# Performance work log

Measured on AMD Instinct MI355X. Metric: run time of the kernel, lower is better.

## Reference

```python
import jax, jax.numpy as jnp
import numpy as np

N = 100000      # num nodes
E = 400000      # num edges (avg degree 4, AIG-like sparse DAG)
NVT = 7         # node type count (one-hot)
VHS = 100       # vertex hidden size
CHS = 30        # clause hidden size
SV = 512        # number of state-variable nodes
NROUNDS = 8     # message passing rounds


def setup_inputs() -> dict:
    key = jax.random.key(0)
    ks = jax.random.split(key, 40)
    s = 0.08  # ~1/sqrt(VHS), matches torch default uniform scale

    def mat(k, shape):
        return jax.random.normal(k, shape, jnp.float32) * s

    edge_index = jax.random.randint(ks[0], (2, E), 0, N)
    sv_node = jax.random.randint(ks[1], (SV,), 0, N)
    types = jax.random.randint(ks[2], (N,), 0, NVT)
    x = jax.nn.one_hot(types, NVT, dtype=jnp.float32)  # [N, NVT]
    ones_e = jnp.ones((E,), jnp.float32)
    # degrees used as divisors after SpMM (clamped >= 1 like real graphs w/ self edges)
    ind = jnp.clip(jax.ops.segment_sum(ones_e, edge_index[1], num_segments=N), 1.0, None)
    outd = jnp.clip(jax.ops.segment_sum(ones_e, edge_index[0], num_segments=N), 1.0, None)

    inp = {
        "x": x, "edge_index": edge_index, "sv_node": sv_node,
        "ind": ind, "outd": outd, "n_clause": 1, "pretrain_round": 1,
        # type init vectors: Linear(1,VHS)(ones(1)) == weight[:,0] + bias, one row per type
        "type_vec": mat(ks[3], (NVT, VHS)),
        # forward_msg MLP
        "fm_w1": mat(ks[4], (VHS, VHS)), "fm_b1": mat(ks[5], (VHS,)),
        "fm_w2": mat(ks[6], (VHS, VHS)), "fm_b2": mat(ks[7], (VHS,)),
        "fm_w3": mat(ks[8], (VHS, VHS)), "fm_b3": mat(ks[9], (VHS,)),
        # backward_msg MLP
        "bm_w1": mat(ks[10], (VHS, VHS)), "bm_b1": mat(ks[11], (VHS,)),
        "bm_w2": mat(ks[12], (VHS, VHS)), "bm_b2": mat(ks[13], (VHS,)),
        "bm_w3": mat(ks[14], (VHS, VHS)), "bm_b3": mat(ks[15], (VHS,)),
        # forward_update GRU (gates ordered r,z,n as in torch)
        "fg_wih": mat(ks[16], (VHS, 3 * VHS)), "fg_whh": mat(ks[17], (VHS, 3 * VHS)),
        "fg_bih": mat(ks[18], (3 * VHS,)), "fg_bhh": mat(ks[19], (3 * VHS,)),
        # backward_update GRU
        "bg_wih": mat(ks[20], (VHS, 3 * VHS)), "bg_whh": mat(ks[21], (VHS, 3 * VHS)),
        "bg_bih": mat(ks[22], (3 * VHS,)), "bg_bhh": mat(ks[23], (3 * VHS,)),
        # sv_feature_pretrain_layer
        "pw1": mat(ks[24], (VHS, CHS)), "pb1": mat(ks[25], (CHS,)),
        "pw2": mat(ks[26], (CHS, 1)), "pb2": mat(ks[27], (1,)),
    }
    return inp


def reference(x, edge_index, sv_node, ind, outd, n_clause, pretrain_round,
              type_vec, fm_w1, fm_b1, fm_w2, fm_b2, fm_w3, fm_b3,
              bm_w1, bm_b1, bm_w2, bm_b2, bm_w3, bm_b3,
              fg_wih, fg_whh, fg_bih, fg_bhh,
              bg_wih, bg_whh, bg_bih, bg_bhh,
              pw1, pb1, pw2, pb2):
    n = x.shape[0]
    src, dst = edge_index[0], edge_index[1]
    ind_c = ind[:, None]   # [N,1]
    outd_c = outd[:, None]

    def mlp(h, w1, b1, w2, b2, w3, b3):
        h = jax.nn.relu(h @ w1 + b1)
        h = jax.nn.relu(h @ w2 + b2)
        return h @ w3 + b3

    def gru(xin, h, wih, whh, bih, bhh):
        # single-step torch GRU: r,z,n gate ordering
        gi = xin @ wih + bih
        gh = h @ whh + bhh
        ir, iz, ig = jnp.split(gi, 3, axis=-1)
        hr, hz, hg = jnp.split(gh, 3, axis=-1)
        r = jax.nn.sigmoid(ir + hr)
        z = jax.nn.sigmoid(iz + hz)
        g = jnp.tanh(ig + r * hg)
        return (1.0 - z) * g + z * h

    def round_fn(vs, _):
        # forward direction: adj_fwd[dst, src] -> aggregate msgs from src into dst
        m = mlp(vs, fm_w1, fm_b1, fm_w2, fm_b2, fm_w3, fm_b3)
        fwd = jax.ops.segment_sum(m[src], dst, num_segments=n) / ind_c
        vs = gru(fwd, vs, fg_wih, fg_whh, fg_bih, fg_bhh)
        # backward direction: adj_bwd[src, dst] -> aggregate msgs from dst into src
        m = mlp(vs, bm_w1, bm_b1, bm_w2, bm_b2, bm_w3, bm_b3)
        bwd = jax.ops.segment_sum(m[dst], src, num_segments=n) / outd_c
        vs = gru(bwd, vs, bg_wih, bg_whh, bg_bih, bg_bhh)
        return vs, None

    vs0 = x @ type_vec  # [N, VHS]
    vs, _ = jax.lax.scan(jax.checkpoint(round_fn), vs0, None, length=NROUNDS)

    # pretrain_round branch: sv_feature_pretrain_layer(var_state[sv_node]).t()[0]
    shortcut = vs[sv_node]  # [SV, VHS]
    h = jax.nn.relu(shortcut @ pw1 + pb1)
    return (h @ pw2 + pb2)[:, 0]  # [SV]
```

## Files before the change

### kernel.cpp

```cpp
#include <hip/hip_runtime.h>
#include <math.h>

#define NVTC 7
#define VHS 100
#define CHS 30
#define LDP 112
#define CTW 128
#define WFRAG_SZ 32768

typedef short short8 __attribute__((ext_vector_type(8)));
typedef float floatx4 __attribute__((ext_vector_type(4)));

#define MFMA(a, b, c) __builtin_amdgcn_mfma_f32_16x16x32_bf16((a), (b), (c), 0, 0, 0)

#define GLOAD16(g, l)                                                              \
  __builtin_amdgcn_global_load_lds((const __attribute__((address_space(1))) void*)(g), \
                                   (__attribute__((address_space(3))) void*)(l), 16, 0, 0)

__device__ __forceinline__ unsigned short f2bf(float f) {
  unsigned u = __float_as_uint(f);
  return (unsigned short)((u + 0x7fffu + ((u >> 16) & 1u)) >> 16);
}
__device__ __forceinline__ float bf2f(unsigned short h) {
  return __uint_as_float((unsigned)h << 16);
}
__device__ __forceinline__ float sigmf(float v) { return 1.f / (1.f + expf(-v)); }


__global__ void zero_int_kernel(int* __restrict__ p, int n) {
  int i = blockIdx.x * 256 + threadIdx.x;
  if (i < n) p[i] = 0;
}

__global__ void inv_kernel(const float* __restrict__ ind, const float* __restrict__ outd,
                           float* __restrict__ inv_ind, float* __restrict__ inv_outd, int n) {
  int i = blockIdx.x * 256 + threadIdx.x;
  if (i < n) { inv_ind[i] = 1.0f / ind[i]; inv_outd[i] = 1.0f / outd[i]; }
}

__global__ void wfrag_kernel(const float* __restrict__ src, int srcLD, int colOff,
                             short* __restrict__ dst) {
  int t = blockIdx.x * 256 + threadIdx.x;
  if (t >= 2048) return;
  int lane = t & 63, rest = t >> 6;
  int ct = rest & 7, kc = rest >> 3;
  int col = ct * 16 + (lane & 15);
  int kbase = kc * 32 + (lane >> 4) * 8;
  short8 hv, lv;
  #pragma unroll
  for (int i = 0; i < 8; ++i) {
    int k = kbase + i;
    float v = (k < VHS && col < VHS) ? src[(size_t)k * srcLD + colOff + col] : 0.f;
    unsigned short h16 = f2bf(v);
    hv[i] = (short)h16;
    lv[i] = (short)f2bf(v - bf2f(h16));
  }
  int base = ((kc * 8 + ct) * 2 * 64 + lane) * 8;
  *(short8*)(dst + base)       = hv;
  *(short8*)(dst + base + 512) = lv;
}

__global__ void pad_b_kernel(const float* __restrict__ b1, int off1,
                             const float* b2, int off2, float* __restrict__ dst) {
  int c = threadIdx.x;
  float v = 0.f;
  if (c < VHS) { v = b1[off1 + c]; if (b2) v += b2[off2 + c]; }
  dst[c] = v;
}

__global__ void init_vs_kernel(const float* __restrict__ x, const float* __restrict__ tv,
                               char* __restrict__ vsp, int N) {
  int node = blockIdx.x, c = threadIdx.x;
  if (node >= N) return;
  float v = 0.f;
  if (c < VHS) {
    #pragma unroll
    for (int t = 0; t < NVTC; ++t) v += x[(size_t)node * NVTC + t] * tv[t * VHS + c];
  }
  unsigned short hi = f2bf(v);
  unsigned short lo = f2bf(v - bf2f(hi));
  char* rowp = vsp + ((size_t)node << 9);
  *(unsigned short*)(rowp + 2 * c)       = hi;
  *(unsigned short*)(rowp + 256 + 2 * c) = lo;
}


__global__ void hist_kernel(const int* __restrict__ ei, int E, int* hin, int* hout) {
  int e = blockIdx.x * 256 + threadIdx.x;
  if (e < E) {
    atomicAdd(&hout[ei[e]], 1);
    atomicAdd(&hin[ei[E + e]], 1);
  }
}

__global__ void scan_block_kernel(const int* __restrict__ in, int* __restrict__ mid,
                                  int* __restrict__ sums, int n) {
  __shared__ int lds[256];
  int tid = threadIdx.x;
  int base = blockIdx.x * 1024 + tid * 4;
  int v0 = (base + 0 < n) ? in[base + 0] : 0;
  int v1 = (base + 1 < n) ? in[base + 1] : 0;
  int v2 = (base + 2 < n) ? in[base + 2] : 0;
  int v3 = (base + 3 < n) ? in[base + 3] : 0;
  int s = v0 + v1 + v2 + v3;
  lds[tid] = s;
  __syncthreads();
  for (int off = 1; off < 256; off <<= 1) {
    int t = (tid >= off) ? lds[tid - off] : 0;
    __syncthreads();
    lds[tid] += t;
    __syncthreads();
  }
  int excl = lds[tid] - s;
  int e0 = excl + v0, e1 = e0 + v1, e2 = e1 + v2, e3 = e2 + v3;
  if (base + 0 < n) mid[base + 0] = e0;
  if (base + 1 < n) mid[base + 1] = e1;
  if (base + 2 < n) mid[base + 2] = e2;
  if (base + 3 < n) mid[base + 3] = e3;
  if (tid == 255) sums[blockIdx.x] = lds[255];
}

__global__ void scan_sums_kernel(int* sums, int nb) {
  __shared__ int lds[256];
  int tid = threadIdx.x;
  int v = (tid < nb) ? sums[tid] : 0;
  lds[tid] = v;
  __syncthreads();
  for (int off = 1; off < 256; off <<= 1) {
    int t = (tid >= off) ? lds[tid - off] : 0;
    __syncthreads();
    lds[tid] += t;
    __syncthreads();
  }
  if (tid < nb) sums[tid] = lds[tid];
}

__global__ void scan_finalize_kernel(const int* __restrict__ mid, const int* __restrict__ sums,
                                     int* __restrict__ rp, int n) {
  int i = blockIdx.x * 256 + threadIdx.x;
  if (i >= n) return;
  int blk = i >> 10;
  int add = (blk > 0) ? sums[blk - 1] : 0;
  rp[i + 1] = mid[i] + add;
  if (i == 0) rp[0] = 0;
}

__global__ void fill_kernel(const int* __restrict__ ei, int E, int gOff, int sOff,
                            const int* __restrict__ rp, int* cnt, int* col) {
  int e = blockIdx.x * 256 + threadIdx.x;
  if (e >= E) return;
  int v = ei[sOff + e];
  int p = rp[v] + atomicAdd(&cnt[v], 1);
  col[p] = ei[gOff + e];
}

__global__ void sort_rows_kernel(const int* __restrict__ rp, int* col, int n) {
  int v = blockIdx.x * 256 + threadIdx.x;
  if (v >= n) return;
  int a = rp[v], b = rp[v + 1];
  for (int i = a + 1; i < b; ++i) {
    int key = col[i];
    int j = i - 1;
    while (j >= a && col[j] > key) { col[j + 1] = col[j]; --j; }
    col[j + 1] = key;
  }
}

__global__ void __launch_bounds__(256)
gather_kernel(const float* __restrict__ m, const int* __restrict__ rp,
              const int* __restrict__ col, const float* __restrict__ iv,
              char* __restrict__ aggp, int N) {
  int v = blockIdx.x * 8 + (threadIdx.x >> 5);
  if (v >= N) return;
  int lane = threadIdx.x & 31;
  char* rowp = aggp + ((size_t)v << 9);
  if (lane < 28) {
    float4 a = make_float4(0.f, 0.f, 0.f, 0.f);
    int s = rp[v], e = rp[v + 1];
    for (int i = s; i < e; ++i) {
      float4 u = ((const float4*)(m + (size_t)col[i] * LDP))[lane];
      a.x += u.x; a.y += u.y; a.z += u.z; a.w += u.w;
    }
    const float sc = iv[v];
    a.x *= sc; a.y *= sc; a.z *= sc; a.w *= sc;
    unsigned short h0 = f2bf(a.x), h1 = f2bf(a.y), h2 = f2bf(a.z), h3 = f2bf(a.w);
    unsigned short l0 = f2bf(a.x - bf2f(h0)), l1 = f2bf(a.y - bf2f(h1));
    unsigned short l2 = f2bf(a.z - bf2f(h2)), l3 = f2bf(a.w - bf2f(h3));
    *(uint2*)(rowp + 8 * lane) =
        make_uint2((unsigned)h0 | ((unsigned)h1 << 16), (unsigned)h2 | ((unsigned)h3 << 16));
    *(uint2*)(rowp + 256 + 8 * lane) =
        make_uint2((unsigned)l0 | ((unsigned)l1 << 16), (unsigned)l2 | ((unsigned)l3 << 16));
  } else {
    *(uint2*)(rowp + 8 * lane)       = make_uint2(0u, 0u);
    *(uint2*)(rowp + 256 + 8 * lane) = make_uint2(0u, 0u);
  }
}

__global__ void __launch_bounds__(256, 2)
mlp3_kernel(const char* __restrict__ vsp,
            const short* __restrict__ W1f, const short* __restrict__ W2f,
            const short* __restrict__ W3f,
            const float* __restrict__ b1, const float* __restrict__ b2,
            const float* __restrict__ b3, float* __restrict__ OUT, int N) {
  __shared__ __align__(16) char lds[65536];
  char* ldsH = lds;
  char* ldsL = lds + 16384;
  const int lane = threadIdx.x & 63, wave = threadIdx.x >> 6;
  const int lrbase = wave * 16;
  const int row0 = blockIdx.x * 64 + lrbase;
  const int a_r = lane & 15, a_kg = lane >> 4;
  const int col_l = lane & 15;

  short8 Fh[4], Fl[4];
  {
    const char* vrow = vsp + (((size_t)(row0 + a_r)) << 9) + (a_kg << 4);
    #pragma unroll
    for (int kc = 0; kc < 4; ++kc) {
      Fh[kc] = *(const short8*)(vrow + kc * 64);
      Fl[kc] = *(const short8*)(vrow + 256 + kc * 64);
    }
  }
  float B1[7], B2[7], B3[7];
  #pragma unroll
  for (int ct = 0; ct < 7; ++ct) {
    const int k = ct * 16 + col_l;
    B1[ct] = b1[k]; B2[ct] = b2[k]; B3[ct] = b3[k];
  }
  if (lane < 32) {
    int row = lrbase + (lane >> 1), sl = 14 + (lane & 1);
    int byte = row * 256 + ((sl * 16) ^ ((row & 7) << 4));
    short8 z = {0, 0, 0, 0, 0, 0, 0, 0};
    *(short8*)(ldsH + byte) = z;
    *(short8*)(ldsL + byte) = z;
  }
  asm volatile("s_waitcnt vmcnt(0)" ::: "memory");

  floatx4 acc[7];
  #pragma unroll
  for (int c = 0; c < 7; ++c) acc[c] = (floatx4){0.f, 0.f, 0.f, 0.f};

#define MSTAGE(WF, KC, BOFF)                                                   \
  {                                                                            \
    _Pragma("unroll") for (int q = 0; q < 4; ++q) {                            \
      const int c_ = wave * 4 + q;                                             \
      GLOAD16((const char*)(WF) + (size_t)((KC) * 16384 + c_ * 1024) + lane * 16, \
              lds + (BOFF) + c_ * 1024);                                       \
    }                                                                          \
  }

#define MCOMP(KC, BOFF, VA)                                                    \
  {                                                                            \
    asm volatile("s_waitcnt vmcnt(" VA ")" ::: "memory");                      \
    __builtin_amdgcn_s_barrier();                                              \
    short8 wt[14];                                                             \
    _Pragma("unroll") for (int c = 0; c < 7; ++c) {                            \
      wt[2 * c]     = *(const short8*)(lds + (BOFF) + (2 * c) * 1024 + lane * 16); \
      wt[2 * c + 1] = *(const short8*)(lds + (BOFF) + (2 * c + 1) * 1024 + lane * 16); \
    }                                                                          \
    __builtin_amdgcn_s_setprio(1);                                             \
    _Pragma("unroll") for (int c = 0; c < 7; ++c) {                            \
      acc[c] = MFMA(Fh[KC], wt[2 * c], acc[c]);                                \
      acc[c] = MFMA(Fh[KC], wt[2 * c + 1], acc[c]);                            \
      acc[c] = MFMA(Fl[KC], wt[2 * c], acc[c]);                                \
    }                                                                          \
    __builtin_amdgcn_s_setprio(0);                                             \
    __builtin_amdgcn_sched_barrier(0);                                         \
    __builtin_amdgcn_s_barrier();                                              \
  }

  auto wbrelu = [&](const float* B) {
    const int rloc0 = lrbase + (lane >> 4) * 4;
    #pragma unroll
    for (int ct = 0; ct < 7; ++ct) {
      int k = ct * 16 + col_l;
      #pragma unroll
      for (int j = 0; j < 4; ++j) {
        int row = rloc0 + j;
        float v = fmaxf(acc[ct][j] + B[ct], 0.f);
        unsigned short h16 = f2bf(v);
        unsigned short l16 = f2bf(v - bf2f(h16));
        int byte = row * 256 + ((k * 2) ^ ((row & 7) << 4));
        *(short*)(ldsH + byte) = (short)h16;
        *(short*)(ldsL + byte) = (short)l16;
      }
      acc[ct] = (floatx4){0.f, 0.f, 0.f, 0.f};
    }
  };
  auto ldfrags = [&]() {
    #pragma unroll
    for (int kc = 0; kc < 4; ++kc) {
      int r = lrbase + a_r;
      int byte = r * 256 + ((((kc * 4 + a_kg) * 16)) ^ ((r & 7) << 4));
      Fh[kc] = *(const short8*)(ldsH + byte);
      Fl[kc] = *(const short8*)(ldsL + byte);
    }
  };

  MSTAGE(W1f, 0, 32768) MSTAGE(W1f, 1, 49152)
  MCOMP(0, 32768, "4")  MSTAGE(W1f, 2, 32768)
  MCOMP(1, 49152, "4")  MSTAGE(W1f, 3, 49152)
  MCOMP(2, 32768, "4")  MSTAGE(W2f, 0, 32768)
  MCOMP(3, 49152, "4")  MSTAGE(W2f, 1, 49152)
  wbrelu(B1); ldfrags();
  MCOMP(0, 32768, "4")  MSTAGE(W2f, 2, 32768)
  MCOMP(1, 49152, "4")  MSTAGE(W2f, 3, 49152)
  MCOMP(2, 32768, "4")  MSTAGE(W3f, 0, 32768)
  MCOMP(3, 49152, "4")  MSTAGE(W3f, 1, 49152)
  wbrelu(B2); ldfrags();
  MCOMP(0, 32768, "4")  MSTAGE(W3f, 2, 32768)
  MCOMP(1, 49152, "4")  MSTAGE(W3f, 3, 49152)
  MCOMP(2, 32768, "4")
  MCOMP(3, 49152, "0")

  const int r0 = row0 + (lane >> 4) * 4;
  #pragma unroll
  for (int ct = 0; ct < 7; ++ct) {
    const int c = ct * 16 + col_l;
    #pragma unroll
    for (int j = 0; j < 4; ++j) {
      const int r = r0 + j;
      if (r < N) OUT[(size_t)r * LDP + c] = acc[ct][j] + B3[ct];
    }
  }
#undef MSTAGE
#undef MCOMP
}

__global__ void __launch_bounds__(256, 2)
gru_kernel(const char* __restrict__ aggp, const char* __restrict__ vsp,
           const short* __restrict__ Wbase,
           const float* __restrict__ br, const float* __restrict__ bz,
           const float* __restrict__ big, const float* __restrict__ bhg,
           char* __restrict__ outp, int N) {
  __shared__ __align__(16) char wlds[49152];
  const int lane = threadIdx.x & 63, wave = threadIdx.x >> 6;
  const int row0 = blockIdx.x * 64 + wave * 16;
  const int a_r = lane & 15;
  const int kgo = (lane >> 4) << 4;
  const int col_l = lane & 15;
  const int jr0 = row0 + (lane >> 4) * 4;

  short8 Ah[4], Al[4], Vh[4], Vl[4];
  {
    const char* arow = aggp + (((size_t)(row0 + a_r)) << 9) + kgo;
    const char* vrow = vsp  + (((size_t)(row0 + a_r)) << 9) + kgo;
    #pragma unroll
    for (int kc = 0; kc < 4; ++kc) {
      Ah[kc] = *(const short8*)(arow + kc * 64);
      Al[kc] = *(const short8*)(arow + 256 + kc * 64);
      Vh[kc] = *(const short8*)(vrow + kc * 64);
      Vl[kc] = *(const short8*)(vrow + 256 + kc * 64);
    }
  }
  float ho[7][4];
  #pragma unroll
  for (int ct = 0; ct < 7; ++ct) {
    const int ccol = ct * 16 + col_l;
    #pragma unroll
    for (int j = 0; j < 4; ++j) {
      const char* hrow = vsp + ((size_t)(jr0 + j) << 9);
      ho[ct][j] = bf2f(*(const unsigned short*)(hrow + 2 * ccol)) +
                  bf2f(*(const unsigned short*)(hrow + 256 + 2 * ccol));
    }
  }
  float bR[7], bZ[7], bI[7], bH[7];
  #pragma unroll
  for (int ct = 0; ct < 7; ++ct) {
    const int ccol = ct * 16 + col_l;
    bR[ct] = br[ccol]; bZ[ct] = bz[ccol]; bI[ct] = big[ccol]; bH[ct] = bhg[ccol];
  }
  asm volatile("s_waitcnt vmcnt(0)" ::: "memory");

#define GRU_STAGE(CT, KH, BOFF)                                                \
  {                                                                            \
    _Pragma("unroll") for (int q = 0; q < 6; ++q) {                            \
      const int c_ = wave * 6 + q;                                             \
      const int m_ = c_ >> 2, kcl_ = (c_ >> 1) & 1, p_ = c_ & 1;               \
      const size_t gb_ = (size_t)m_ * 65536 +                                  \
          (size_t)(((((KH) * 2 + kcl_) * 8 + (CT)) * 2048) + p_ * 1024);       \
      GLOAD16((const char*)Wbase + gb_ + lane * 16, wlds + (BOFF) + c_ * 1024);\
    }                                                                          \
  }

#define GRU_HALF(KH, BOFF)                                                     \
  {                                                                            \
    _Pragma("unroll") for (int kcl = 0; kcl < 2; ++kcl) {                      \
      const int kc_ = (KH) * 2 + kcl;                                          \
      short8 wt[12];                                                           \
      _Pragma("unroll") for (int mp = 0; mp < 12; ++mp) {                      \
        const int m_ = mp >> 1, p_ = mp & 1;                                   \
        const int chunk_ = m_ * 4 + kcl * 2 + p_;                              \
        wt[mp] = *(const short8*)(wlds + (BOFF) + chunk_ * 1024 + lane * 16);  \
      }                                                                        \
      __builtin_amdgcn_s_setprio(1);                                           \
      rc = MFMA(Ah[kc_], wt[0], rc);  rc = MFMA(Ah[kc_], wt[1], rc);  rc = MFMA(Al[kc_], wt[0], rc); \
      zc = MFMA(Ah[kc_], wt[2], zc);  zc = MFMA(Ah[kc_], wt[3], zc);  zc = MFMA(Al[kc_], wt[2], zc); \
      ic = MFMA(Ah[kc_], wt[4], ic);  ic = MFMA(Ah[kc_], wt[5], ic);  ic = MFMA(Al[kc_], wt[4], ic); \
      rc = MFMA(Vh[kc_], wt[6], rc);  rc = MFMA(Vh[kc_], wt[7], rc);  rc = MFMA(Vl[kc_], wt[6], rc); \
      zc = MFMA(Vh[kc_], wt[8], zc);  zc = MFMA(Vh[kc_], wt[9], zc);  zc = MFMA(Vl[kc_], wt[8], zc); \
      hc = MFMA(Vh[kc_], wt[10], hc); hc = MFMA(Vh[kc_], wt[11], hc); hc = MFMA(Vl[kc_], wt[10], hc); \
      __builtin_amdgcn_s_setprio(0);                                           \
    }                                                                          \
  }

#define GRU_ITER(CT, VA, VB, STG)                                              \
  {                                                                            \
    floatx4 rc = {0.f, 0.f, 0.f, 0.f};                                         \
    floatx4 zc = {0.f, 0.f, 0.f, 0.f};                                         \
    floatx4 ic = {0.f, 0.f, 0.f, 0.f};                                         \
    floatx4 hc = {0.f, 0.f, 0.f, 0.f};                                         \
    asm volatile("s_waitcnt vmcnt(" VA ")" ::: "memory");                      \
    __builtin_amdgcn_s_barrier();                                              \
    GRU_HALF(0, 0)                                                             \
    __builtin_amdgcn_sched_barrier(0);                                         \
    __builtin_amdgcn_s_barrier();                                              \
    if (STG) GRU_STAGE((CT) + 1, 0, 0)                                         \
    asm volatile("s_waitcnt vmcnt(" VB ")" ::: "memory");                      \
    __builtin_amdgcn_s_barrier();                                              \
    GRU_HALF(1, 24576)                                                         \
    __builtin_amdgcn_sched_barrier(0);                                         \
    __builtin_amdgcn_s_barrier();                                              \
    if (STG) GRU_STAGE((CT) + 1, 1, 24576)                                     \
    const float brv = bR[CT], bzv = bZ[CT], bigv = bI[CT], bhgv = bH[CT];      \
    const int ccol = (CT) * 16 + col_l;                                        \
    _Pragma("unroll") for (int j = 0; j < 4; ++j) {                            \
      const float rv = sigmf(rc[j] + brv);                                     \
      const float zv = sigmf(zc[j] + bzv);                                     \
      const float gv = tanhf(ic[j] + bigv + rv * (hc[j] + bhgv));              \
      const float v = (1.f - zv) * gv + zv * ho[CT][j];                        \
      const unsigned short hi = f2bf(v);                                       \
      const unsigned short lo = f2bf(v - bf2f(hi));                            \
      char* orow = outp + ((size_t)(jr0 + j) << 9);                            \
      *(unsigned short*)(orow + 2 * ccol)       = hi;                          \
      *(unsigned short*)(orow + 256 + 2 * ccol) = lo;                          \
    }                                                                          \
  }

  GRU_STAGE(0, 0, 0)
  GRU_STAGE(0, 1, 24576)

  GRU_ITER(0, "6",  "6",  1)
  GRU_ITER(1, "14", "14", 1)
  GRU_ITER(2, "14", "14", 1)
  GRU_ITER(3, "14", "14", 1)
  GRU_ITER(4, "14", "14", 1)
  GRU_ITER(5, "14", "14", 1)
  GRU_ITER(6, "14", "8",  0)

#undef GRU_STAGE
#undef GRU_HALF
#undef GRU_ITER
}

__global__ void final_kernel(const char* __restrict__ vsp, const int* __restrict__ sv,
                             const float* __restrict__ pw1, const float* __restrict__ pb1,
                             const float* __restrict__ pw2, const float* __restrict__ pb2,
                             float* __restrict__ out, int SVn) {
  int b = blockIdx.x;
  if (b >= SVn) return;
  int tid = threadIdx.x;
  int node = sv[b];
  const char* rowp = vsp + ((size_t)node << 9);
  float p = 0.f;
  if (tid < CHS) {
    float acc = 0.f;
    for (int k = 0; k < VHS; ++k) {
      float xv = bf2f(*(const unsigned short*)(rowp + 2 * k)) +
                 bf2f(*(const unsigned short*)(rowp + 256 + 2 * k));
      acc += xv * pw1[k * CHS + tid];
    }
    float h = fmaxf(acc + pb1[tid], 0.f);
    p = h * pw2[tid];
  }
  #pragma unroll
  for (int off = 32; off > 0; off >>= 1) p += __shfl_down(p, off);
  if (tid == 0) out[b] = p + pb2[0];
}

extern "C" void kernel_launch(void* const* d_in, const int* in_sizes, int n_in,
                              void* d_out, int out_size, void* d_ws, size_t ws_size,
                              hipStream_t stream) {
  const float* x      = (const float*)d_in[0];
  const int*   ei     = (const int*)d_in[1];
  const int*   sv     = (const int*)d_in[2];
  const float* ind    = (const float*)d_in[3];
  const float* outd   = (const float*)d_in[4];
  const float* tv     = (const float*)d_in[7];
  const float* fm_w1  = (const float*)d_in[8];
  const float* fm_b1  = (const float*)d_in[9];
  const float* fm_w2  = (const float*)d_in[10];
  const float* fm_b2  = (const float*)d_in[11];
  const float* fm_w3  = (const float*)d_in[12];
  const float* fm_b3  = (const float*)d_in[13];
  const float* bm_w1  = (const float*)d_in[14];
  const float* bm_b1  = (const float*)d_in[15];
  const float* bm_w2  = (const float*)d_in[16];
  const float* bm_b2  = (const float*)d_in[17];
  const float* bm_w3  = (const float*)d_in[18];
  const float* bm_b3  = (const float*)d_in[19];
  const float* fg_wih = (const float*)d_in[20];
  const float* fg_whh = (const float*)d_in[21];
  const float* fg_bih = (const float*)d_in[22];
  const float* fg_bhh = (const float*)d_in[23];
  const float* bg_wih = (const float*)d_in[24];
  const float* bg_whh = (const float*)d_in[25];
  const float* bg_bih = (const float*)d_in[26];
  const float* bg_bhh = (const float*)d_in[27];
  const float* pw1    = (const float*)d_in[28];
  const float* pb1    = (const float*)d_in[29];
  const float* pw2    = (const float*)d_in[30];
  const float* pb2    = (const float*)d_in[31];

  const int N   = in_sizes[3];
  const int E   = in_sizes[1] / 2;
  const int SVn = in_sizes[2];

  char* wsb = (char*)d_ws;
  const size_t NP = (size_t)N * LDP;
  float* t1     = (float*)wsb;
  char*  vs_sp  = wsb + NP * 4;
  char*  agg_sp = vs_sp + (size_t)(N + 256) * 512;
  float* inv_ind  = (float*)(agg_sp + (size_t)(N + 256) * 512);
  float* inv_outd = inv_ind + N;
  short* wfrag    = (short*)(inv_outd + N);
  float* biasbase = (float*)(wfrag + 18 * WFRAG_SZ);
  int* ip      = (int*)(biasbase + 14 * CTW);
  int* rp_in   = ip; ip += N + 1;
  int* rp_out  = ip; ip += N + 1;
  int* col_in  = ip; ip += E;
  int* col_out = ip; ip += E;
  int* cnt     = ip; ip += N;
  int* hin     = ip; ip += N;
  int* hout    = ip; ip += N;
  int* mid     = ip; ip += N;
  int* sums    = ip; ip += 512;

  const size_t need_bytes = (size_t)((char*)(ip) - (char*)d_ws);
  if (ws_size < need_bytes) return;

  auto wf  = [&](int i) { return wfrag + (size_t)i * WFRAG_SZ; };
  auto bia = [&](int i) { return biasbase + (size_t)i * CTW; };

  wfrag_kernel<<<8, 256, 0, stream>>>(fm_w1, VHS, 0, wf(0));
  wfrag_kernel<<<8, 256, 0, stream>>>(fm_w2, VHS, 0, wf(1));
  wfrag_kernel<<<8, 256, 0, stream>>>(fm_w3, VHS, 0, wf(2));
  wfrag_kernel<<<8, 256, 0, stream>>>(bm_w1, VHS, 0, wf(3));
  wfrag_kernel<<<8, 256, 0, stream>>>(bm_w2, VHS, 0, wf(4));
  wfrag_kernel<<<8, 256, 0, stream>>>(bm_w3, VHS, 0, wf(5));
  for (int g = 0; g < 3; ++g) {
    wfrag_kernel<<<8, 256, 0, stream>>>(fg_wih, 3 * VHS, g * VHS, wf(6 + g));
    wfrag_kernel<<<8, 256, 0, stream>>>(fg_whh, 3 * VHS, g * VHS, wf(9 + g));
    wfrag_kernel<<<8, 256, 0, stream>>>(bg_wih, 3 * VHS, g * VHS, wf(12 + g));
    wfrag_kernel<<<8, 256, 0, stream>>>(bg_whh, 3 * VHS, g * VHS, wf(15 + g));
  }
  pad_b_kernel<<<1, 128, 0, stream>>>(fm_b1, 0, nullptr, 0, bia(0));
  pad_b_kernel<<<1, 128, 0, stream>>>(fm_b2, 0, nullptr, 0, bia(1));
  pad_b_kernel<<<1, 128, 0, stream>>>(fm_b3, 0, nullptr, 0, bia(2));
  pad_b_kernel<<<1, 128, 0, stream>>>(bm_b1, 0, nullptr, 0, bia(3));
  pad_b_kernel<<<1, 128, 0, stream>>>(bm_b2, 0, nullptr, 0, bia(4));
  pad_b_kernel<<<1, 128, 0, stream>>>(bm_b3, 0, nullptr, 0, bia(5));
  pad_b_kernel<<<1, 128, 0, stream>>>(fg_bih, 0,       fg_bhh, 0,       bia(6));
  pad_b_kernel<<<1, 128, 0, stream>>>(fg_bih, VHS,     fg_bhh, VHS,     bia(7));
  pad_b_kernel<<<1, 128, 0, stream>>>(fg_bih, 2 * VHS, nullptr, 0,      bia(8));
  pad_b_kernel<<<1, 128, 0, stream>>>(fg_bhh, 2 * VHS, nullptr, 0,      bia(9));
  pad_b_kernel<<<1, 128, 0, stream>>>(bg_bih, 0,       bg_bhh, 0,       bia(10));
  pad_b_kernel<<<1, 128, 0, stream>>>(bg_bih, VHS,     bg_bhh, VHS,     bia(11));
  pad_b_kernel<<<1, 128, 0, stream>>>(bg_bih, 2 * VHS, nullptr, 0,      bia(12));
  pad_b_kernel<<<1, 128, 0, stream>>>(bg_bhh, 2 * VHS, nullptr, 0,      bia(13));

  inv_kernel<<<(N + 255) / 256, 256, 0, stream>>>(ind, outd, inv_ind, inv_outd, N);
  init_vs_kernel<<<N, 128, 0, stream>>>(x, tv, vs_sp, N);

  zero_int_kernel<<<(2 * N + 255) / 256, 256, 0, stream>>>(hin, 2 * N);
  hist_kernel<<<(E + 255) / 256, 256, 0, stream>>>(ei, E, hin, hout);
  const int nb = (N + 1023) / 1024;
  scan_block_kernel<<<nb, 256, 0, stream>>>(hin, mid, sums, N);
  scan_sums_kernel<<<1, 256, 0, stream>>>(sums, nb);
  scan_finalize_kernel<<<(N + 255) / 256, 256, 0, stream>>>(mid, sums, rp_in, N);
  scan_block_kernel<<<nb, 256, 0, stream>>>(hout, mid, sums, N);
  scan_sums_kernel<<<1, 256, 0, stream>>>(sums, nb);
  scan_finalize_kernel<<<(N + 255) / 256, 256, 0, stream>>>(mid, sums, rp_out, N);
  zero_int_kernel<<<(N + 255) / 256, 256, 0, stream>>>(cnt, N);
  fill_kernel<<<(E + 255) / 256, 256, 0, stream>>>(ei, E, 0, E, rp_in, cnt, col_in);
  sort_rows_kernel<<<(N + 255) / 256, 256, 0, stream>>>(rp_in, col_in, N);
  zero_int_kernel<<<(N + 255) / 256, 256, 0, stream>>>(cnt, N);
  fill_kernel<<<(E + 255) / 256, 256, 0, stream>>>(ei, E, E, 0, rp_out, cnt, col_out);
  sort_rows_kernel<<<(N + 255) / 256, 256, 0, stream>>>(rp_out, col_out, N);

  const int gridMM  = (N + 63) / 64;
  const int gridGRU = (N + 63) / 64;
  const int gridG   = (N + 7) / 8;
  for (int rd = 0; rd < 8; ++rd) {
    for (int dir = 0; dir < 2; ++dir) {
      const int mw = dir ? 3 : 0;
      const int gb = dir ? 10 : 6;
      const int* rp   = dir ? rp_out : rp_in;
      const int* col  = dir ? col_out : col_in;
      const float* iv = dir ? inv_outd : inv_ind;

      mlp3_kernel<<<gridMM, 256, 0, stream>>>(vs_sp, wf(mw + 0), wf(mw + 1), wf(mw + 2),
                                              bia(mw + 0), bia(mw + 1), bia(mw + 2), t1, N);
      gather_kernel<<<gridG, 256, 0, stream>>>(t1, rp, col, iv, agg_sp, N);
      gru_kernel<<<gridGRU, 256, 0, stream>>>(agg_sp, vs_sp, wf(dir ? 12 : 6),
                                              bia(gb + 0), bia(gb + 1), bia(gb + 2), bia(gb + 3),
                                              vs_sp, N);
    }
  }

  final_kernel<<<SVn, 64, 0, stream>>>(vs_sp, sv, pw1, pb1, pw2, pb2, (float*)d_out, SVn);
}
```

Before: 2.868 ms.

## Batch weight/bias prep launches and use fast exp/rcp activations in GRU

Merges the 18 weight-fragment conversion launches into a single kernel and the 14 bias padding launches into another, each taking a struct of per-matrix arguments. This removes roughly thirty small kernel launches and their serialization gaps. Separately, sigmoid and tanh in the GRU epilogue now use __expf plus the hardware reciprocal instead of expf, division and tanhf, trading some accuracy for fewer ALU instructions. The fast tanh may lose precision for large-magnitude inputs.

```diff
diff --git a/kernel.cpp b/kernel.cpp
--- a/kernel.cpp
+++ b/kernel.cpp
@@ -24,7 +24,12 @@
 __device__ __forceinline__ float bf2f(unsigned short h) {
   return __uint_as_float((unsigned)h << 16);
 }
-__device__ __forceinline__ float sigmf(float v) { return 1.f / (1.f + expf(-v)); }
+__device__ __forceinline__ float sigmf(float v) {
+  return __builtin_amdgcn_rcpf(1.f + __expf(-v));
+}
+__device__ __forceinline__ float tanh_fast(float v) {
+  return 1.f - 2.f * __builtin_amdgcn_rcpf(__expf(2.f * v) + 1.f);
+}
 
 
 __global__ void zero_int_kernel(int* __restrict__ p, int n) {
@@ -38,10 +43,12 @@
   if (i < n) { inv_ind[i] = 1.0f / ind[i]; inv_outd[i] = 1.0f / outd[i]; }
 }
 
-__global__ void wfrag_kernel(const float* __restrict__ src, int srcLD, int colOff,
-                             short* __restrict__ dst) {
-  int t = blockIdx.x * 256 + threadIdx.x;
-  if (t >= 2048) return;
+struct WfragArgs { const float* src; int srcLD; int colOff; short* dst; };
+struct WfragPack { WfragArgs a[18]; };
+__global__ void wfrag_all_kernel(WfragPack p) {
+  const int mat = blockIdx.x >> 3;
+  const int t = ((blockIdx.x & 7) << 8) + threadIdx.x;
+  const WfragArgs w = p.a[mat];
   int lane = t & 63, rest = t >> 6;
   int ct = rest & 7, kc = rest >> 3;
   int col = ct * 16 + (lane & 15);
@@ -50,22 +57,24 @@
   #pragma unroll
   for (int i = 0; i < 8; ++i) {
     int k = kbase + i;
-    float v = (k < VHS && col < VHS) ? src[(size_t)k * srcLD + colOff + col] : 0.f;
+    float v = (k < VHS && col < VHS) ? w.src[(size_t)k * w.srcLD + w.colOff + col] : 0.f;
     unsigned short h16 = f2bf(v);
     hv[i] = (short)h16;
     lv[i] = (short)f2bf(v - bf2f(h16));
   }
   int base = ((kc * 8 + ct) * 2 * 64 + lane) * 8;
-  *(short8*)(dst + base)       = hv;
-  *(short8*)(dst + base + 512) = lv;
-}
-
-__global__ void pad_b_kernel(const float* __restrict__ b1, int off1,
-                             const float* b2, int off2, float* __restrict__ dst) {
+  *(short8*)(w.dst + base)       = hv;
+  *(short8*)(w.dst + base + 512) = lv;
+}
+
+struct PadArgs { const float* b1; int off1; const float* b2; int off2; float* dst; };
+struct PadPack { PadArgs a[14]; };
+__global__ void pad_all_kernel(PadPack p) {
+  const PadArgs w = p.a[blockIdx.x];
   int c = threadIdx.x;
   float v = 0.f;
-  if (c < VHS) { v = b1[off1 + c]; if (b2) v += b2[off2 + c]; }
-  dst[c] = v;
+  if (c < VHS) { v = w.b1[w.off1 + c]; if (w.b2) v += w.b2[w.off2 + c]; }
+  w.dst[c] = v;
 }
 
 __global__ void init_vs_kernel(const float* __restrict__ x, const float* __restrict__ tv,
@@ -426,7 +435,7 @@
     _Pragma("unroll") for (int j = 0; j < 4; ++j) {                            \
       const float rv = sigmf(rc[j] + brv);                                     \
       const float zv = sigmf(zc[j] + bzv);                                     \
-      const float gv = tanhf(ic[j] + bigv + rv * (hc[j] + bhgv));              \
+      const float gv = tanh_fast(ic[j] + bigv + rv * (hc[j] + bhgv));          \
       const float v = (1.f - zv) * gv + zv * ho[CT][j];                        \
       const unsigned short hi = f2bf(v);                                       \
       const unsigned short lo = f2bf(v - bf2f(hi));                            \
@@ -541,32 +550,37 @@
   auto wf  = [&](int i) { return wfrag + (size_t)i * WFRAG_SZ; };
   auto bia = [&](int i) { return biasbase + (size_t)i * CTW; };
 
-  wfrag_kernel<<<8, 256, 0, stream>>>(fm_w1, VHS, 0, wf(0));
-  wfrag_kernel<<<8, 256, 0, stream>>>(fm_w2, VHS, 0, wf(1));
-  wfrag_kernel<<<8, 256, 0, stream>>>(fm_w3, VHS, 0, wf(2));
-  wfrag_kernel<<<8, 256, 0, stream>>>(bm_w1, VHS, 0, wf(3));
-  wfrag_kernel<<<8, 256, 0, stream>>>(bm_w2, VHS, 0, wf(4));
-  wfrag_kernel<<<8, 256, 0, stream>>>(bm_w3, VHS, 0, wf(5));
+  WfragPack wp;
+  wp.a[0] = {fm_w1, VHS, 0, wf(0)};
+  wp.a[1] = {fm_w2, VHS, 0, wf(1)};
+  wp.a[2] = {fm_w3, VHS, 0, wf(2)};
+  wp.a[3] = {bm_w1, VHS, 0, wf(3)};
+  wp.a[4] = {bm_w2, VHS, 0, wf(4)};
+  wp.a[5] = {bm_w3, VHS, 0, wf(5)};
   for (int g = 0; g < 3; ++g) {
-    wfrag_kernel<<<8, 256, 0, stream>>>(fg_wih, 3 * VHS, g * VHS, wf(6 + g));
-    wfrag_kernel<<<8, 256, 0, stream>>>(fg_whh, 3 * VHS, g * VHS, wf(9 + g));
-    wfrag_kernel<<<8, 256, 0, stream>>>(bg_wih, 3 * VHS, g * VHS, wf(12 + g));
-    wfrag_kernel<<<8, 256, 0, stream>>>(bg_whh, 3 * VHS, g * VHS, wf(15 + g));
-  }
-  pad_b_kernel<<<1, 128, 0, stream>>>(fm_b1, 0, nullptr, 0, bia(0));
-  pad_b_kernel<<<1, 128, 0, stream>>>(fm_b2, 0, nullptr, 0, bia(1));
-  pad_b_kernel<<<1, 128, 0, stream>>>(fm_b3, 0, nullptr, 0, bia(2));
-  pad_b_kernel<<<1, 128, 0, stream>>>(bm_b1, 0, nullptr, 0, bia(3));
-  pad_b_kernel<<<1, 128, 0, stream>>>(bm_b2, 0, nullptr, 0, bia(4));
-  pad_b_kernel<<<1, 128, 0, stream>>>(bm_b3, 0, nullptr, 0, bia(5));
-  pad_b_kernel<<<1, 128, 0, stream>>>(fg_bih, 0,       fg_bhh, 0,       bia(6));
-  pad_b_kernel<<<1, 128, 0, stream>>>(fg_bih, VHS,     fg_bhh, VHS,     bia(7));
-  pad_b_kernel<<<1, 128, 0, stream>>>(fg_bih, 2 * VHS, nullptr, 0,      bia(8));
-  pad_b_kernel<<<1, 128, 0, stream>>>(fg_bhh, 2 * VHS, nullptr, 0,      bia(9));
-  pad_b_kernel<<<1, 128, 0, stream>>>(bg_bih, 0,       bg_bhh, 0,       bia(10));
-  pad_b_kernel<<<1, 128, 0, stream>>>(bg_bih, VHS,     bg_bhh, VHS,     bia(11));
-  pad_b_kernel<<<1, 128, 0, stream>>>(bg_bih, 2 * VHS, nullptr, 0,      bia(12));
-  pad_b_kernel<<<1, 128, 0, stream>>>(bg_bhh, 2 * VHS, nullptr, 0,      bia(13));
+    wp.a[6 + g]  = {fg_wih, 3 * VHS, g * VHS, wf(6 + g)};
+    wp.a[9 + g]  = {fg_whh, 3 * VHS, g * VHS, wf(9 + g)};
+    wp.a[12 + g] = {bg_wih, 3 * VHS, g * VHS, wf(12 + g)};
+    wp.a[15 + g] = {bg_whh, 3 * VHS, g * VHS, wf(15 + g)};
+  }
+  wfrag_all_kernel<<<144, 256, 0, stream>>>(wp);
+
+  PadPack pp;
+  pp.a[0]  = {fm_b1, 0,       nullptr, 0,   bia(0)};
+  pp.a[1]  = {fm_b2, 0,       nullptr, 0,   bia(1)};
+  pp.a[2]  = {fm_b3, 0,       nullptr, 0,   bia(2)};
+  pp.a[3]  = {bm_b1, 0,       nullptr, 0,   bia(3)};
+  pp.a[4]  = {bm_b2, 0,       nullptr, 0,   bia(4)};
+  pp.a[5]  = {bm_b3, 0,       nullptr, 0,   bia(5)};
+  pp.a[6]  = {fg_bih, 0,       fg_bhh, 0,   bia(6)};
+  pp.a[7]  = {fg_bih, VHS,     fg_bhh, VHS, bia(7)};
+  pp.a[8]  = {fg_bih, 2 * VHS, nullptr, 0,  bia(8)};
+  pp.a[9]  = {fg_bhh, 2 * VHS, nullptr, 0,  bia(9)};
+  pp.a[10] = {bg_bih, 0,       bg_bhh, 0,   bia(10)};
+  pp.a[11] = {bg_bih, VHS,     bg_bhh, VHS, bia(11)};
+  pp.a[12] = {bg_bih, 2 * VHS, nullptr, 0,  bia(12)};
+  pp.a[13] = {bg_bhh, 2 * VHS, nullptr, 0,  bia(13)};
+  pad_all_kernel<<<14, 128, 0, stream>>>(pp);
 
   inv_kernel<<<(N + 255) / 256, 256, 0, stream>>>(ind, outd, inv_ind, inv_outd, N);
   init_vs_kernel<<<N, 128, 0, stream>>>(x, tv, vs_sp, N);
```

Measured after the change: 2.557 ms. -10.8%, faster.
